# Performance work log

Hardware: AMD Instinct MI355X
Metric: run time of the kernel (lower is better)

Reference implementation:

```python
import jax, jax.numpy as jnp
import numpy as np

N_NODES = 100000
N_EDGES = 1600000
F_IN = 64
HID = 64
N_CLASSES = 47


def lgconv(x, src, dst, n_nodes):
    # PyG LGConv: symmetric gcn_norm WITHOUT self-loops, sum aggregation.
    ones = jnp.ones(src.shape[0], dtype=x.dtype)
    deg = jax.ops.segment_sum(ones, dst, num_segments=n_nodes)  # in-degree at targets
    dinv = jnp.where(deg > 0, jax.lax.rsqrt(jnp.maximum(deg, 1.0)), 0.0)
    norm = dinv[src] * dinv[dst]  # [E]
    msg = x[src] * norm[:, None]  # [E, F] gathered messages
    return jax.ops.segment_sum(msg, dst, num_segments=n_nodes)  # [N, F]


def setup_inputs() -> dict:
    key = jax.random.key(0)
    k1, k2, k3, k4 = jax.random.split(key, 4)
    x = jax.random.normal(k1, (N_NODES, F_IN), dtype=jnp.float32)
    edge_index = jax.random.randint(k2, (2, N_EDGES), 0, N_NODES, dtype=jnp.int64)
    W1 = jax.random.normal(k3, (F_IN, HID), dtype=jnp.float32) * (1.0 / np.sqrt(F_IN))
    b1 = jnp.zeros((HID,), dtype=jnp.float32)
    W2 = jax.random.normal(k4, (HID, N_CLASSES), dtype=jnp.float32) * (1.0 / np.sqrt(HID))
    b2 = jnp.zeros((N_CLASSES,), dtype=jnp.float32)
    return {"x": x, "edge_index": edge_index, "W1": W1, "b1": b1, "W2": W2, "b2": b2}


def reference(x, edge_index, W1, b1, W2, b2):
    src, dst = edge_index[0], edge_index[1]
    h = jax.nn.relu(lgconv(x, src, dst, N_NODES))          # conv1 + relu (dropout = id in eval)
    h = jax.nn.relu(h @ W1 + b1)                           # lin1 + relu
    h = jax.nn.relu(lgconv(h, src, dst, N_NODES))          # conv2 + relu
    logits = h @ W2 + b2                                   # lin2
    return jax.nn.log_softmax(logits, axis=-1)
```

## Files before the change

### kernel.cpp

```cpp
#include <hip/hip_runtime.h>
#include <hip/hip_fp16.h>
#include <math.h>

#define NN 100000
#define F 64
#define NC 47
#define NSUP 98
#define SUPR 1024
#define ACHUNK 4096
#define PAD 24576

__global__ __launch_bounds__(256) void binA_direct_kernel(const void* __restrict__ ei,
                                                          int* __restrict__ superCnt,
                                                          unsigned* __restrict__ superArr,
                                                          int E) {
    __shared__ int2 ed[ACHUNK];
    __shared__ int h[128], gbase[128];
    __shared__ int is64_s;
    int t = threadIdx.x;
    if (t < 64) {
        int v = ((const int*)ei)[2 * t + 1];
        unsigned long long ball = __ballot(v == 0);
        if (t == 0) is64_s = (ball == ~0ULL) ? 1 : 0;
    }
    if (t < 128) h[t] = 0;
    __syncthreads();
    bool is64 = (is64_s != 0);
    int cb = blockIdx.x * ACHUNK;
    int ce = min(cb + ACHUNK, E);
    for (int i = cb + t; i < ce; i += 256) {
        int s, d;
        if (is64) {
            s = (int)((const long long*)ei)[i];
            d = (int)((const long long*)ei)[(size_t)E + i];
        } else {
            s = ((const int*)ei)[i];
            d = ((const int*)ei)[(size_t)E + i];
        }
        ed[i - cb] = make_int2(s, d);
        atomicAdd(&h[d >> 10], 1);
    }
    __syncthreads();
    if (t < 128) {
        int c = h[t];
        gbase[t] = (t < NSUP && c > 0) ? atomicAdd(&superCnt[t], c) : 0;
        h[t] = 0;
    }
    __syncthreads();
    int nloc = ce - cb;
    for (int i = t; i < nloc; i += 256) {
        int2 e = ed[i];
        int sup = e.y >> 10;
        int pos = atomicAdd(&h[sup], 1);
        unsigned pk = (unsigned)e.x | ((unsigned)(e.y & (SUPR - 1)) << 17);
        superArr[(size_t)sup * PAD + gbase[sup] + pos] = pk;
    }
}

__global__ __launch_bounds__(1024) void binB_fused_kernel(const unsigned* __restrict__ superArr,
                                                          const int* __restrict__ superCnt,
                                                          int* __restrict__ rowptr,
                                                          float* __restrict__ dinv,
                                                          unsigned* __restrict__ esrc, int E) {
    __shared__ int hist[SUPR];
    __shared__ int sc[SUPR];
    __shared__ int wb_s;
    int s = blockIdx.x, t = threadIdx.x;
    if (t == 0) {
        int r = 0;
        for (int i = 0; i < s; ++i) r += superCnt[i];
        wb_s = r;
    }
    hist[t] = 0;
    __syncthreads();
    int wb = wb_s;
    int cnt = superCnt[s];
    const unsigned* arr = superArr + (size_t)s * PAD;
    int gr = s * SUPR + t;
    for (int i = t; i < cnt; i += 1024)
        atomicAdd(&hist[(arr[i] >> 17) & (SUPR - 1)], 1);
    __syncthreads();
    int myv = hist[t];
    sc[t] = myv;
    __syncthreads();
    for (int off = 1; off < 1024; off <<= 1) {
        int a = (t >= off) ? sc[t - off] : 0;
        __syncthreads();
        sc[t] += a;
        __syncthreads();
    }
    int excl = sc[t] - myv;
    if (gr < NN) {
        rowptr[gr] = wb + excl;
        dinv[gr] = (myv > 0) ? rsqrtf((float)myv) : 0.0f;
    }
    if (s == NSUP - 1 && t == 0) rowptr[NN] = E;
    __syncthreads();
    hist[t] = excl;
    __syncthreads();
    for (int i = t; i < cnt; i += 1024) {
        unsigned e = arr[i];
        int r = (e >> 17) & (SUPR - 1);
        int pos = atomicAdd(&hist[r], 1);
        esrc[wb + pos] = e & 0x1FFFFu;
    }
}

__global__ void f2h_scale_kernel(const float4* __restrict__ in4,
                                 const float* __restrict__ dinv,
                                 uint2* __restrict__ outh, int n4) {
    int i = blockIdx.x * blockDim.x + threadIdx.x;
    if (i >= n4) return;
    float dv = dinv[i >> 4];
    float4 v = in4[i];
    __half2 h01 = __floats2half2_rn(v.x * dv, v.y * dv);
    __half2 h23 = __floats2half2_rn(v.z * dv, v.w * dv);
    uint2 r;
    r.x = *(const unsigned*)&h01;
    r.y = *(const unsigned*)&h23;
    outh[i] = r;
}

__global__ __launch_bounds__(256) void conv_ps_kernel(const uint2* __restrict__ xh,
                                                      const int* __restrict__ rowptr,
                                                      const unsigned* __restrict__ esrc,
                                                      const float* __restrict__ dinv,
                                                      uint2* __restrict__ outh, int n) {
    int row = blockIdx.x * 4 + (threadIdx.x >> 6);
    if (row >= n) return;
    int lane = threadIdx.x & 63;
    int es = lane >> 4, f4 = lane & 15;
    int beg = rowptr[row], end = rowptr[row + 1];
    float4 acc = make_float4(0.f, 0.f, 0.f, 0.f);
    for (int base = beg; base < end; base += 64) {
        int m = end - base;
        if (m > 64) m = 64;
        int pk = (lane < m) ? (int)esrc[base + lane] : 0;
        int iters = (m + 3) >> 2;
        int k = 0;
        for (; k + 4 <= iters; k += 4) {
            int i0 = 4 * k + es, i1 = i0 + 4, i2 = i0 + 8, i3 = i0 + 12;
            int s0 = __shfl(pk, i0, 64);
            int s1 = __shfl(pk, i1, 64);
            int s2 = __shfl(pk, i2, 64);
            int s3 = __shfl(pk, i3, 64);
            float w0 = (i0 < m) ? 1.0f : 0.0f;
            float w1 = (i1 < m) ? 1.0f : 0.0f;
            float w2 = (i2 < m) ? 1.0f : 0.0f;
            float w3 = (i3 < m) ? 1.0f : 0.0f;
            uint2 v0 = xh[(size_t)s0 * 16 + f4];
            uint2 v1 = xh[(size_t)s1 * 16 + f4];
            uint2 v2 = xh[(size_t)s2 * 16 + f4];
            uint2 v3 = xh[(size_t)s3 * 16 + f4];
            float2 a01 = __half22float2(*reinterpret_cast<const __half2*>(&v0.x));
            float2 a23 = __half22float2(*reinterpret_cast<const __half2*>(&v0.y));
            acc.x = fmaf(a01.x, w0, acc.x); acc.y = fmaf(a01.y, w0, acc.y);
            acc.z = fmaf(a23.x, w0, acc.z); acc.w = fmaf(a23.y, w0, acc.w);
            float2 b01 = __half22float2(*reinterpret_cast<const __half2*>(&v1.x));
            float2 b23 = __half22float2(*reinterpret_cast<const __half2*>(&v1.y));
            acc.x = fmaf(b01.x, w1, acc.x); acc.y = fmaf(b01.y, w1, acc.y);
            acc.z = fmaf(b23.x, w1, acc.z); acc.w = fmaf(b23.y, w1, acc.w);
            float2 c01 = __half22float2(*reinterpret_cast<const __half2*>(&v2.x));
            float2 c23 = __half22float2(*reinterpret_cast<const __half2*>(&v2.y));
            acc.x = fmaf(c01.x, w2, acc.x); acc.y = fmaf(c01.y, w2, acc.y);
            acc.z = fmaf(c23.x, w2, acc.z); acc.w = fmaf(c23.y, w2, acc.w);
            float2 d01 = __half22float2(*reinterpret_cast<const __half2*>(&v3.x));
            float2 d23 = __half22float2(*reinterpret_cast<const __half2*>(&v3.y));
            acc.x = fmaf(d01.x, w3, acc.x); acc.y = fmaf(d01.y, w3, acc.y);
            acc.z = fmaf(d23.x, w3, acc.z); acc.w = fmaf(d23.y, w3, acc.w);
        }
        for (; k < iters; ++k) {
            int i0 = 4 * k + es;
            int s0 = __shfl(pk, i0, 64);
            float w0 = (i0 < m) ? 1.0f : 0.0f;
            uint2 v0 = xh[(size_t)s0 * 16 + f4];
            float2 a01 = __half22float2(*reinterpret_cast<const __half2*>(&v0.x));
            float2 a23 = __half22float2(*reinterpret_cast<const __half2*>(&v0.y));
            acc.x = fmaf(a01.x, w0, acc.x); acc.y = fmaf(a01.y, w0, acc.y);
            acc.z = fmaf(a23.x, w0, acc.z); acc.w = fmaf(a23.y, w0, acc.w);
        }
    }
#pragma unroll
    for (int off = 16; off <= 32; off <<= 1) {
        acc.x += __shfl_xor(acc.x, off, 64);
        acc.y += __shfl_xor(acc.y, off, 64);
        acc.z += __shfl_xor(acc.z, off, 64);
        acc.w += __shfl_xor(acc.w, off, 64);
    }
    if (es == 0) {
        float dv = dinv[row];
        __half2 h01 = __floats2half2_rn(acc.x * dv, acc.y * dv);
        __half2 h23 = __floats2half2_rn(acc.z * dv, acc.w * dv);
        uint2 r;
        r.x = *(const unsigned*)&h01;
        r.y = *(const unsigned*)&h23;
        outh[(size_t)row * 16 + f4] = r;
    }
}

__device__ __forceinline__ float4 h4_to_f4_relu(uint2 hv) {
    float2 a01 = __half22float2(*reinterpret_cast<const __half2*>(&hv.x));
    float2 a23 = __half22float2(*reinterpret_cast<const __half2*>(&hv.y));
    return make_float4(fmaxf(a01.x, 0.f), fmaxf(a01.y, 0.f),
                       fmaxf(a23.x, 0.f), fmaxf(a23.y, 0.f));
}

__global__ __launch_bounds__(256) void lin1_kernel(const uint2* __restrict__ h2,
                                                   const float* __restrict__ W1,
                                                   const float* __restrict__ b1,
                                                   const float* __restrict__ dinv,
                                                   __half* __restrict__ outh, int n) {
    __shared__ float wt[64 * 64];
    __shared__ float ht[64 * 64];
    int t = threadIdx.x;
    for (int i = t; i < 64 * 64; i += 256) {
        int k = i >> 6, c = i & 63;
        int kq = k >> 2, slot = kq ^ (c & 7);
        wt[c * 64 + slot * 4 + (k & 3)] = W1[i];
    }
    int row0 = blockIdx.x * 64;
    float4* ht4 = (float4*)ht;
#pragma unroll
    for (int j = 0; j < 4; ++j) {
        int flat = t + 256 * j;
        int r = flat >> 4;
        int kq = flat & 15;
        int gr = row0 + r;
        float4 v = (gr < n) ? h4_to_f4_relu(h2[(size_t)gr * 16 + kq])
                            : make_float4(0.f, 0.f, 0.f, 0.f);
        ht4[r * 16 + (kq ^ ((r >> 2) & 7))] = v;
    }
    __syncthreads();
    const float4* wt4 = (const float4*)wt;
    const float4* ht4c = (const float4*)ht;

    int tx = t & 15, ty = t >> 4;
    float acc[4][4] = {};
#pragma unroll 2
    for (int kq = 0; kq < 16; ++kq) {
        int wslot = kq ^ (tx & 7);
        float4 b0 = wt4[(tx +  0) * 16 + wslot];
        float4 b1v = wt4[(tx + 16) * 16 + wslot];
        float4 b2v = wt4[(tx + 32) * 16 + wslot];
        float4 b3v = wt4[(tx + 48) * 16 + wslot];
        int aslot = kq ^ (ty & 7);
#pragma unroll
        for (int i = 0; i < 4; ++i) {
            float4 a = ht4c[(4 * ty + i) * 16 + aslot];
            acc[i][0] = fmaf(a.x, b0.x,  fmaf(a.y, b0.y,  fmaf(a.z, b0.z,  fmaf(a.w, b0.w,  acc[i][0]))));
            acc[i][1] = fmaf(a.x, b1v.x, fmaf(a.y, b1v.y, fmaf(a.z, b1v.z, fmaf(a.w, b1v.w, acc[i][1]))));
            acc[i][2] = fmaf(a.x, b2v.x, fmaf(a.y, b2v.y, fmaf(a.z, b2v.z, fmaf(a.w, b2v.w, acc[i][2]))));
            acc[i][3] = fmaf(a.x, b3v.x, fmaf(a.y, b3v.y, fmaf(a.z, b3v.z, fmaf(a.w, b3v.w, acc[i][3]))));
        }
    }
    float bj[4];
#pragma unroll
    for (int g = 0; g < 4; ++g) bj[g] = b1[tx + 16 * g];
    int r0 = row0 + 4 * ty;
#pragma unroll
    for (int i = 0; i < 4; ++i) {
        int r = r0 + i;
        if (r >= n) break;
        float dv = dinv[r];
#pragma unroll
        for (int g = 0; g < 4; ++g)
            outh[(size_t)r * 64 + tx + 16 * g] =
                __float2half(fmaxf(acc[i][g] + bj[g], 0.0f) * dv);
    }
}

__global__ __launch_bounds__(256) void lin2_kernel(const uint2* __restrict__ h2,
                                                   const float* __restrict__ W2,
                                                   const float* __restrict__ b2,
                                                   float* __restrict__ out, int n) {
    __shared__ float wt[64 * 64];
    __shared__ float ht[64 * 64];
    int t = threadIdx.x;
    for (int i = t; i < 64 * 64; i += 256) {
        int k = i >> 6, c = i & 63;
        int kq = k >> 2, slot = kq ^ (c & 7);
        wt[c * 64 + slot * 4 + (k & 3)] = (c < NC) ? W2[k * NC + c] : 0.0f;
    }
    int row0 = blockIdx.x * 64;
    float4* ht4 = (float4*)ht;
#pragma unroll
    for (int j = 0; j < 4; ++j) {
        int flat = t + 256 * j;
        int r = flat >> 4;
        int kq = flat & 15;
        int gr = row0 + r;
        float4 v = (gr < n) ? h4_to_f4_relu(h2[(size_t)gr * 16 + kq])
                            : make_float4(0.f, 0.f, 0.f, 0.f);
        ht4[r * 16 + (kq ^ ((r >> 2) & 7))] = v;
    }
    __syncthreads();
    const float4* wt4 = (const float4*)wt;
    const float4* ht4c = (const float4*)ht;

    int tx = t & 15, ty = t >> 4;
    float acc[4][4] = {};
#pragma unroll 2
    for (int kq = 0; kq < 16; ++kq) {
        int wslot = kq ^ (tx & 7);
        float4 b0 = wt4[(tx +  0) * 16 + wslot];
        float4 b1v = wt4[(tx + 16) * 16 + wslot];
        float4 b2v = wt4[(tx + 32) * 16 + wslot];
        float4 b3v = wt4[(tx + 48) * 16 + wslot];
        int aslot = kq ^ (ty & 7);
#pragma unroll
        for (int i = 0; i < 4; ++i) {
            float4 a = ht4c[(4 * ty + i) * 16 + aslot];
            acc[i][0] = fmaf(a.x, b0.x,  fmaf(a.y, b0.y,  fmaf(a.z, b0.z,  fmaf(a.w, b0.w,  acc[i][0]))));
            acc[i][1] = fmaf(a.x, b1v.x, fmaf(a.y, b1v.y, fmaf(a.z, b1v.z, fmaf(a.w, b1v.w, acc[i][1]))));
            acc[i][2] = fmaf(a.x, b2v.x, fmaf(a.y, b2v.y, fmaf(a.z, b2v.z, fmaf(a.w, b2v.w, acc[i][2]))));
            acc[i][3] = fmaf(a.x, b3v.x, fmaf(a.y, b3v.y, fmaf(a.z, b3v.z, fmaf(a.w, b3v.w, acc[i][3]))));
        }
    }
    bool vm[4];
    float bj[4];
#pragma unroll
    for (int g = 0; g < 4; ++g) {
        int c = tx + 16 * g;
        vm[g] = (c < NC);
        bj[g] = vm[g] ? b2[c] : 0.0f;
    }
    int r0 = row0 + 4 * ty;
#pragma unroll
    for (int i = 0; i < 4; ++i) {
        int r = r0 + i;
        float v[4];
        float m = -INFINITY;
#pragma unroll
        for (int g = 0; g < 4; ++g) {
            v[g] = acc[i][g] + bj[g];
            if (vm[g]) m = fmaxf(m, v[g]);
        }
#pragma unroll
        for (int off = 8; off > 0; off >>= 1) m = fmaxf(m, __shfl_xor(m, off, 64));
        float s = 0.0f;
#pragma unroll
        for (int g = 0; g < 4; ++g)
            if (vm[g]) s += expf(v[g] - m);
#pragma unroll
        for (int off = 8; off > 0; off >>= 1) s += __shfl_xor(s, off, 64);
        float lse = m + logf(s);
        if (r < n) {
#pragma unroll
            for (int g = 0; g < 4; ++g)
                if (vm[g]) out[(size_t)r * NC + tx + 16 * g] = v[g] - lse;
        }
    }
}

extern "C" void kernel_launch(void* const* d_in, const int* in_sizes, int n_in,
                              void* d_out, int out_size, void* d_ws, size_t ws_size,
                              hipStream_t stream) {
    const float* x  = (const float*)d_in[0];
    const void*  ei = d_in[1];
    const float* W1 = (const float*)d_in[2];
    const float* b1 = (const float*)d_in[3];
    const float* W2 = (const float*)d_in[4];
    const float* b2 = (const float*)d_in[5];
    float* out = (float*)d_out;

    const int E = in_sizes[1] / 2;

    char* ws = (char*)d_ws;
    size_t off = 0;
    auto alloc = [&](size_t bytes) -> void* {
        void* p = ws + off;
        off = (off + bytes + 255) & ~(size_t)255;
        return p;
    };
    float*    dinv      = (float*)   alloc((size_t)NN * 4);
    int*      superCnt  = (int*)     alloc(128 * 4);
    unsigned* superArr  = (unsigned*)alloc((size_t)NSUP * PAD * 4);
    int*      rowptr    = (int*)     alloc((size_t)(NN + 1) * 4);
    unsigned* esrc      = (unsigned*)alloc((size_t)E * 4);
    uint2*    xh        = (uint2*)   alloc((size_t)NN * 16 * 8);
    __half*   bufAh     = (__half*)  alloc((size_t)NN * F * 2);
    __half*   bufBh     = (__half*)  alloc((size_t)NN * F * 2);

    hipMemsetAsync(superCnt, 0, 128 * 4, stream);

    binA_direct_kernel<<<(E + ACHUNK - 1) / ACHUNK, 256, 0, stream>>>(
        ei, superCnt, superArr, E);
    binB_fused_kernel<<<NSUP, 1024, 0, stream>>>(
        superArr, superCnt, rowptr, dinv, esrc, E);

    f2h_scale_kernel<<<(NN * 16 + 255) / 256, 256, 0, stream>>>(
        (const float4*)x, dinv, xh, NN * 16);

    const int conv_blocks = (NN + 3) / 4;
    const int lin_blocks = (NN + 63) / 64;

    conv_ps_kernel<<<conv_blocks, 256, 0, stream>>>(xh, rowptr, esrc, dinv,
                                                    (uint2*)bufAh, NN);

    lin1_kernel<<<lin_blocks, 256, 0, stream>>>((const uint2*)bufAh, W1, b1, dinv,
                                                bufBh, NN);

    conv_ps_kernel<<<conv_blocks, 256, 0, stream>>>((const uint2*)bufBh, rowptr, esrc,
                                                    dinv, (uint2*)bufAh, NN);

    lin2_kernel<<<lin_blocks, 256, 0, stream>>>((const uint2*)bufAh, W2, b2, out, NN);
}
```

Measured before the change: 181.1 us.

## Use finer super-buckets with separate superscan and wave-shuffle binB kernel

Shrinks super-buckets from 1024 to 256 destination rows, giving 391 binB blocks of 256 threads instead of 98 blocks of 1024. This spreads the second binning pass over more CUs. A new single-block kernel computes the super-bucket base offsets once, replacing the serial per-block prefix loop, and the in-block scan now uses wave shuffles. The cost is an extra kernel launch and more global atomics on superCnt in binA. PAD of 5120 against an expected ~4096 edges per bucket could overflow on skewed degree distributions.

```diff
diff --git a/kernel.cpp b/kernel.cpp
--- a/kernel.cpp
+++ b/kernel.cpp
@@ -5,17 +5,17 @@
 #define NN 100000
 #define F 64
 #define NC 47
-#define NSUP 98
-#define SUPR 1024
+#define NSUP 391
+#define SUPR 256
 #define ACHUNK 4096
-#define PAD 24576
+#define PAD 5120
 
 __global__ __launch_bounds__(256) void binA_direct_kernel(const void* __restrict__ ei,
                                                           int* __restrict__ superCnt,
                                                           unsigned* __restrict__ superArr,
                                                           int E) {
     __shared__ int2 ed[ACHUNK];
-    __shared__ int h[128], gbase[128];
+    __shared__ int h[512], gbase[512];
     __shared__ int is64_s;
     int t = threadIdx.x;
     if (t < 64) {
@@ -23,7 +23,7 @@
         unsigned long long ball = __ballot(v == 0);
         if (t == 0) is64_s = (ball == ~0ULL) ? 1 : 0;
     }
-    if (t < 128) h[t] = 0;
+    h[t] = 0; h[t + 256] = 0;
     __syncthreads();
     bool is64 = (is64_s != 0);
     int cb = blockIdx.x * ACHUNK;
@@ -38,70 +38,89 @@
             d = ((const int*)ei)[(size_t)E + i];
         }
         ed[i - cb] = make_int2(s, d);
-        atomicAdd(&h[d >> 10], 1);
-    }
-    __syncthreads();
-    if (t < 128) {
-        int c = h[t];
-        gbase[t] = (t < NSUP && c > 0) ? atomicAdd(&superCnt[t], c) : 0;
-        h[t] = 0;
+        atomicAdd(&h[d >> 8], 1);
+    }
+    __syncthreads();
+    for (int b = t; b < 512; b += 256) {
+        int c = h[b];
+        gbase[b] = (b < NSUP && c > 0) ? atomicAdd(&superCnt[b], c) : 0;
+        h[b] = 0;
     }
     __syncthreads();
     int nloc = ce - cb;
     for (int i = t; i < nloc; i += 256) {
         int2 e = ed[i];
-        int sup = e.y >> 10;
+        int sup = e.y >> 8;
         int pos = atomicAdd(&h[sup], 1);
         unsigned pk = (unsigned)e.x | ((unsigned)(e.y & (SUPR - 1)) << 17);
         superArr[(size_t)sup * PAD + gbase[sup] + pos] = pk;
     }
 }
 
-__global__ __launch_bounds__(1024) void binB_fused_kernel(const unsigned* __restrict__ superArr,
-                                                          const int* __restrict__ superCnt,
-                                                          int* __restrict__ rowptr,
-                                                          float* __restrict__ dinv,
-                                                          unsigned* __restrict__ esrc, int E) {
-    __shared__ int hist[SUPR];
-    __shared__ int sc[SUPR];
-    __shared__ int wb_s;
-    int s = blockIdx.x, t = threadIdx.x;
-    if (t == 0) {
-        int r = 0;
-        for (int i = 0; i < s; ++i) r += superCnt[i];
-        wb_s = r;
-    }
-    hist[t] = 0;
-    __syncthreads();
-    int wb = wb_s;
-    int cnt = superCnt[s];
-    const unsigned* arr = superArr + (size_t)s * PAD;
-    int gr = s * SUPR + t;
-    for (int i = t; i < cnt; i += 1024)
-        atomicAdd(&hist[(arr[i] >> 17) & (SUPR - 1)], 1);
-    __syncthreads();
-    int myv = hist[t];
-    sc[t] = myv;
-    __syncthreads();
-    for (int off = 1; off < 1024; off <<= 1) {
+__global__ __launch_bounds__(512) void superscan_kernel(const int* __restrict__ superCnt,
+                                                        int* __restrict__ superBase) {
+    __shared__ int sc[512];
+    int t = threadIdx.x;
+    int v = (t < NSUP) ? superCnt[t] : 0;
+    sc[t] = v;
+    __syncthreads();
+    for (int off = 1; off < 512; off <<= 1) {
         int a = (t >= off) ? sc[t - off] : 0;
         __syncthreads();
         sc[t] += a;
         __syncthreads();
     }
-    int excl = sc[t] - myv;
+    if (t < NSUP) superBase[t] = sc[t] - v;
+    if (t == NSUP - 1) superBase[NSUP] = sc[t];
+}
+
+__global__ __launch_bounds__(256) void binB_kernel(const unsigned* __restrict__ superArr,
+                                                   const int* __restrict__ superCnt,
+                                                   const int* __restrict__ superBase,
+                                                   int* __restrict__ rowptr,
+                                                   float* __restrict__ dinv,
+                                                   unsigned* __restrict__ esrc, int E) {
+    __shared__ int hist[256];
+    __shared__ int cur[256];
+    __shared__ int wsum[4], wbase[4];
+    int s = blockIdx.x, t = threadIdx.x;
+    int wb = superBase[s];
+    int cnt = superCnt[s];
+    const unsigned* arr = superArr + (size_t)s * PAD;
+    hist[t] = 0;
+    __syncthreads();
+    for (int i = t; i < cnt; i += 256)
+        atomicAdd(&hist[(arr[i] >> 17) & (SUPR - 1)], 1);
+    __syncthreads();
+    int myv = hist[t];
+    int lane = t & 63, w = t >> 6;
+    int v = myv;
+#pragma unroll
+    for (int off = 1; off < 64; off <<= 1) {
+        int u = __shfl_up(v, off, 64);
+        if (lane >= off) v += u;
+    }
+    if (lane == 63) wsum[w] = v;
+    __syncthreads();
+    if (t == 0) {
+        int r = 0;
+#pragma unroll
+        for (int j = 0; j < 4; ++j) { wbase[j] = r; r += wsum[j]; }
+    }
+    __syncthreads();
+    int excl = v + wbase[w] - myv;
+    int gr = s * SUPR + t;
     if (gr < NN) {
         rowptr[gr] = wb + excl;
         dinv[gr] = (myv > 0) ? rsqrtf((float)myv) : 0.0f;
     }
     if (s == NSUP - 1 && t == 0) rowptr[NN] = E;
-    __syncthreads();
-    hist[t] = excl;
-    __syncthreads();
-    for (int i = t; i < cnt; i += 1024) {
+    cur[t] = excl;
+    __syncthreads();
+    for (int i = t; i < cnt; i += 256) {
         unsigned e = arr[i];
         int r = (e >> 17) & (SUPR - 1);
-        int pos = atomicAdd(&hist[r], 1);
+        int pos = atomicAdd(&cur[r], 1);
         esrc[wb + pos] = e & 0x1FFFFu;
     }
 }
@@ -373,7 +392,8 @@
         return p;
     };
     float*    dinv      = (float*)   alloc((size_t)NN * 4);
-    int*      superCnt  = (int*)     alloc(128 * 4);
+    int*      superCnt  = (int*)     alloc(512 * 4);
+    int*      superBase = (int*)     alloc(512 * 4);
     unsigned* superArr  = (unsigned*)alloc((size_t)NSUP * PAD * 4);
     int*      rowptr    = (int*)     alloc((size_t)(NN + 1) * 4);
     unsigned* esrc      = (unsigned*)alloc((size_t)E * 4);
@@ -381,12 +401,13 @@
     __half*   bufAh     = (__half*)  alloc((size_t)NN * F * 2);
     __half*   bufBh     = (__half*)  alloc((size_t)NN * F * 2);
 
-    hipMemsetAsync(superCnt, 0, 128 * 4, stream);
+    hipMemsetAsync(superCnt, 0, 512 * 4, stream);
 
     binA_direct_kernel<<<(E + ACHUNK - 1) / ACHUNK, 256, 0, stream>>>(
         ei, superCnt, superArr, E);
-    binB_fused_kernel<<<NSUP, 1024, 0, stream>>>(
-        superArr, superCnt, rowptr, dinv, esrc, E);
+    superscan_kernel<<<1, 512, 0, stream>>>(superCnt, superBase);
+    binB_kernel<<<NSUP, 256, 0, stream>>>(
+        superArr, superCnt, superBase, rowptr, dinv, esrc, E);
 
     f2h_scale_kernel<<<(NN * 16 + 255) / 256, 256, 0, stream>>>(
         (const float4*)x, dinv, xh, NN * 16);
```

Result: no change. 180.0 us (-0.6%).
